# Performance work log

Hardware: AMD Instinct MI355X
Metric: run time of the kernel (lower is better)

The kernel has to match this reference:

```python
import jax, jax.numpy as jnp
import numpy as np

DIM = 128
HEADS = 4
OUT = DIM // HEADS  # 32
NEG_SLOPE = 0.2
EPS = 1e-16


def setup_inputs() -> dict:
    key = jax.random.key(0)
    k1, k2, k3, k4, k5, k6 = jax.random.split(key, 6)
    B, T, E = 4, 4096, 131072
    x = jax.random.normal(k1, (B, T, DIM), dtype=jnp.float32)
    edge_index = jax.random.randint(k2, (2, E), 0, T, dtype=jnp.int64)
    # GATConv params (PyG layout): lin weight [heads*out, in], att [heads, out], bias [heads*out]
    W = jax.random.normal(k3, (HEADS * OUT, DIM), dtype=jnp.float32) / np.sqrt(DIM)
    att_src = jax.random.normal(k4, (HEADS, OUT), dtype=jnp.float32) / np.sqrt(OUT)
    att_dst = jax.random.normal(k5, (HEADS, OUT), dtype=jnp.float32) / np.sqrt(OUT)
    bias = jax.random.normal(k6, (HEADS * OUT,), dtype=jnp.float32) * 0.01
    return {"x": x, "edge_index": edge_index, "W": W, "att_src": att_src, "att_dst": att_dst, "bias": bias}


def reference(x, edge_index, W, att_src, att_dst, bias):
    B, T, D = x.shape
    N = B * T
    E = edge_index.shape[1]
    # batch the temporal edge list: repeat(1, B) + per-graph node offset b*T
    offsets = jnp.repeat(jnp.arange(B, dtype=edge_index.dtype) * T, E)
    src = jnp.tile(edge_index[0], B) + offsets
    dst = jnp.tile(edge_index[1], B) + offsets
    # PyG GATConv default add_self_loops=True
    loops = jnp.arange(N, dtype=edge_index.dtype)
    src = jnp.concatenate([src, loops])
    dst = jnp.concatenate([dst, loops])

    h = (x.reshape(N, D) @ W.T).reshape(N, HEADS, OUT)          # [N,H,O]
    a_src = jnp.einsum('nho,ho->nh', h, att_src)                # [N,H]
    a_dst = jnp.einsum('nho,ho->nh', h, att_dst)

    e = a_src[src] + a_dst[dst]                                  # [Etot,H]
    e = jax.nn.leaky_relu(e, NEG_SLOPE)
    # segment softmax over destination neighborhoods
    m = jax.ops.segment_max(e, dst, num_segments=N)              # [N,H]
    ex = jnp.exp(e - m[dst])
    s = jax.ops.segment_sum(ex, dst, num_segments=N)
    alpha = ex / (s[dst] + EPS)                                  # [Etot,H]

    msg = h[src] * alpha[:, :, None]                             # [Etot,H,O]
    out = jax.ops.segment_sum(msg, dst, num_segments=N)          # [N,H,O]
    out = out.reshape(N, HEADS * OUT) + bias
    return out.reshape(B, T, D)
```

## Files before the change

kernel.cpp:

```cpp
#include <hip/hip_runtime.h>

#define TPG   4096
#define NHEAD 4
#define DIMD  128
#define NEG   0.2f

__device__ __forceinline__ int load_edge(const void* ei, int is64, long idx) {
  if (is64) return (int)((const long long*)ei)[idx];
  return ((const int*)ei)[idx];
}

__device__ __forceinline__ int detect64_block(const unsigned* __restrict__ ei) {
  __shared__ int s64;
  int t = threadIdx.x;
  if (t == 0) s64 = 1;
  __syncthreads();
  if (t < 256) {
    unsigned v = ei[2 * t + 1];
    if (v != 0u) s64 = 0;
  }
  __syncthreads();
  return s64;
}

__global__ __launch_bounds__(256) void k_gemm(
    const float* __restrict__ x, const float* __restrict__ W,
    const float* __restrict__ atts, const float* __restrict__ attd,
    float* __restrict__ h, float* __restrict__ as_n, float* __restrict__ ad_n,
    int* __restrict__ counts) {
  __shared__ float4 xs4[16][33];
  int t = threadIdx.x;
  if (blockIdx.x < 16) counts[(blockIdx.x << 8) + t] = 0;
  int base = blockIdx.x * 16;
  const float4* x4 = (const float4*)x;
  for (int i = t; i < 512; i += 256) {
    xs4[i >> 5][i & 31] = x4[base * 32 + i];
  }
  __syncthreads();

  int n_sub = t & 15, cgrp = t >> 4;
  int c0 = cgrp * 8;
  const float4* W4 = (const float4*)W;
  float acc[8];
#pragma unroll
  for (int k = 0; k < 8; ++k) acc[k] = 0.f;

  for (int db = 0; db < 32; db += 8) {
    float4 xa[8];
#pragma unroll
    for (int i = 0; i < 8; ++i) xa[i] = xs4[n_sub][db + i];
#pragma unroll
    for (int k = 0; k < 8; ++k) {
      const float4* wr = W4 + (c0 + k) * 32 + db;
      float a = acc[k];
#pragma unroll
      for (int i = 0; i < 8; ++i) {
        float4 w = wr[i];
        a = fmaf(xa[i].x, w.x, a);
        a = fmaf(xa[i].y, w.y, a);
        a = fmaf(xa[i].z, w.z, a);
        a = fmaf(xa[i].w, w.w, a);
      }
      acc[k] = a;
    }
  }

  int n = base + n_sub;
  float4* hp = (float4*)(h + (n << 7) + c0);
  hp[0] = make_float4(acc[0], acc[1], acc[2], acc[3]);
  hp[1] = make_float4(acc[4], acc[5], acc[6], acc[7]);

  float ps = 0.f, pd = 0.f;
#pragma unroll
  for (int k = 0; k < 8; ++k) {
    ps = fmaf(acc[k], atts[c0 + k], ps);
    pd = fmaf(acc[k], attd[c0 + k], pd);
  }
  ps += __shfl_xor(ps, 16); ps += __shfl_xor(ps, 32);
  pd += __shfl_xor(pd, 16); pd += __shfl_xor(pd, 32);
  if ((t & 48) == 0) {
    as_n[(n << 2) + (t >> 6)] = ps;
    ad_n[(n << 2) + (t >> 6)] = pd;
  }
}

__global__ __launch_bounds__(256) void k_hist(const void* __restrict__ ei,
                                              int* __restrict__ counts, int E) {
  int is64 = detect64_block((const unsigned*)ei);
  int e = blockIdx.x * blockDim.x + threadIdx.x;
  if (e >= E) return;
  int dst = load_edge(ei, is64, (long)E + e);
  atomicAdd(&counts[dst], 1);
}

__global__ __launch_bounds__(1024) void k_scan(const int* __restrict__ counts,
                                               int* __restrict__ offs,
                                               int* __restrict__ cursor) {
  __shared__ int wsum[16];
  __shared__ int woff[17];
  int t = threadIdx.x;
  int b = t * 4;
  int v0 = counts[b], v1 = counts[b + 1], v2 = counts[b + 2], v3 = counts[b + 3];
  int s0 = v0 + v1 + v2 + v3;
  int lane = t & 63, w = t >> 6;
  int sc = s0;
#pragma unroll
  for (int off = 1; off < 64; off <<= 1) {
    int o = __shfl_up(sc, off);
    if (lane >= off) sc += o;
  }
  if (lane == 63) wsum[w] = sc;
  __syncthreads();
  if (t == 0) {
    int a = 0;
#pragma unroll
    for (int i = 0; i < 16; ++i) { woff[i] = a; a += wsum[i]; }
    woff[16] = a;
  }
  __syncthreads();
  int a = woff[w] + sc - s0;
  offs[b] = a;     cursor[b] = a;     a += v0;
  offs[b + 1] = a; cursor[b + 1] = a; a += v1;
  offs[b + 2] = a; cursor[b + 2] = a; a += v2;
  offs[b + 3] = a; cursor[b + 3] = a;
  if (t == 1023) offs[4096] = woff[16];
}

__global__ __launch_bounds__(256) void k_scatter(const void* __restrict__ ei,
                                                 int* __restrict__ cursor,
                                                 int* __restrict__ esrc, int E) {
  int is64 = detect64_block((const unsigned*)ei);
  int e = blockIdx.x * blockDim.x + threadIdx.x;
  if (e >= E) return;
  int src = load_edge(ei, is64, e);
  int dst = load_edge(ei, is64, (long)E + e);
  int pos = atomicAdd(&cursor[dst], 1);
  esrc[pos] = src;
}

__global__ __launch_bounds__(256) void k_aggr(
    const int* __restrict__ offs, const int* __restrict__ esrc,
    const float* __restrict__ h, const float* __restrict__ as_n,
    const float* __restrict__ ad_n, const float* __restrict__ bias,
    float* __restrict__ out) {
  int lane = threadIdx.x & 63;
  int n = __builtin_amdgcn_readfirstlane((blockIdx.x << 2) + (threadIdx.x >> 6));
  int tloc = n & (TPG - 1);
  int nodebase = n - tloc;
  int beg = __builtin_amdgcn_readfirstlane(offs[tloc]);
  int end = __builtin_amdgcn_readfirstlane(offs[tloc + 1]);

  int myh = lane >> 4;
  int c = lane << 1;
  float adst = ad_n[(n << 2) + myh];

  float m, s;
  float2 acc;
  {
    float e = as_n[(n << 2) + myh] + adst;
    e = e > 0.f ? e : NEG * e;
    m = e; s = 1.f;
    acc = *(const float2*)(h + ((size_t)n << 7) + c);
  }

  for (int j0 = beg; j0 < end; j0 += 8) {
    int sgk[8];
#pragma unroll
    for (int k = 0; k < 8; ++k) {
      int j = j0 + k;
      sgk[k] = (j < end) ? (nodebase + esrc[j]) : n;
    }
    float ek[8];
#pragma unroll
    for (int k = 0; k < 8; ++k) {
      float e = as_n[((size_t)sgk[k] << 2) + myh] + adst;
      e = e > 0.f ? e : NEG * e;
      ek[k] = (j0 + k < end) ? e : -1e30f;
    }
    float2 hv[8];
#pragma unroll
    for (int k = 0; k < 8; ++k)
      hv[k] = *(const float2*)(h + ((size_t)sgk[k] << 7) + c);

    float bm = ek[0];
#pragma unroll
    for (int k = 1; k < 8; ++k) bm = fmaxf(bm, ek[k]);
    float mn = fmaxf(m, bm);
    float r = __expf(m - mn);
    float ps = 0.f, px = 0.f, py = 0.f;
#pragma unroll
    for (int k = 0; k < 8; ++k) {
      float al = __expf(ek[k] - mn);
      ps += al;
      px = fmaf(al, hv[k].x, px);
      py = fmaf(al, hv[k].y, py);
    }
    acc.x = fmaf(acc.x, r, px);
    acc.y = fmaf(acc.y, r, py);
    s = fmaf(s, r, ps);
    m = mn;
  }

  float invs = 1.f / (s + 1e-16f);
  const float2 bi = *(const float2*)(bias + c);
  float2 o;
  o.x = fmaf(acc.x, invs, bi.x);
  o.y = fmaf(acc.y, invs, bi.y);
  *(float2*)(out + ((size_t)n << 7) + c) = o;
}

extern "C" void kernel_launch(void* const* d_in, const int* in_sizes, int n_in,
                              void* d_out, int out_size, void* d_ws, size_t ws_size,
                              hipStream_t stream) {
  const float* x    = (const float*)d_in[0];
  const void*  ei   = d_in[1];
  const float* W    = (const float*)d_in[2];
  const float* atts = (const float*)d_in[3];
  const float* attd = (const float*)d_in[4];
  const float* bias = (const float*)d_in[5];
  float* out = (float*)d_out;

  int N = in_sizes[0] / DIMD;
  int E = in_sizes[1] / 2;

  char* p = (char*)d_ws;
  float* h      = (float*)p; p += (size_t)N * DIMD * 4;
  float* as_n   = (float*)p; p += (size_t)N * NHEAD * 4;
  float* ad_n   = (float*)p; p += (size_t)N * NHEAD * 4;
  int*   counts = (int*)p;   p += (size_t)TPG * 4;
  int*   offs   = (int*)p;   p += (size_t)(TPG + 1) * 4;
  int*   cursor = (int*)p;   p += (size_t)TPG * 4;
  int*   esrc   = (int*)p;   p += (size_t)E * 4;

  k_gemm<<<N / 16, 256, 0, stream>>>(x, W, atts, attd, h, as_n, ad_n, counts);
  k_hist<<<(E + 255) / 256, 256, 0, stream>>>(ei, counts, E);
  k_scan<<<1, 1024, 0, stream>>>(counts, offs, cursor);
  k_scatter<<<(E + 255) / 256, 256, 0, stream>>>(ei, cursor, esrc, E);
  k_aggr<<<N / 4, 256, 0, stream>>>(offs, esrc, h, as_n, ad_n, bias, out);
}
```

Before: 153.2 us.

## Fuse histogram and scan via last-block pattern, remap aggregation to two waves per node

The separate scan launch is folded into the histogram kernel: the last block to finish, detected through an atomic counter reset in the GEMM kernel, performs the prefix sum over destination counts. The aggregation kernel now uses two wavefronts per node, each handling two heads with one float per lane instead of float2. Blocks are remapped so that each batch graph's nodes are grouped onto a pair of XCDs, aiming at better L2 locality for h gathers. This removes one launch and raises parallelism, at the cost of more redundant index/logit loads per node and a serialized tail block for the scan.

Result: slower. 170.6 us (+11.4%).

```diff
diff --git a/kernel.cpp b/kernel.cpp
--- a/kernel.cpp
+++ b/kernel.cpp
@@ -27,10 +27,11 @@
     const float* __restrict__ x, const float* __restrict__ W,
     const float* __restrict__ atts, const float* __restrict__ attd,
     float* __restrict__ h, float* __restrict__ as_n, float* __restrict__ ad_n,
-    int* __restrict__ counts) {
+    int* __restrict__ counts, int* __restrict__ done) {
   __shared__ float4 xs4[16][33];
   int t = threadIdx.x;
   if (blockIdx.x < 16) counts[(blockIdx.x << 8) + t] = 0;
+  if (blockIdx.x == 16 && t == 0) *done = 0;
   int base = blockIdx.x * 16;
   const float4* x4 = (const float4*)x;
   for (int i = t; i < 512; i += 256) {
@@ -66,7 +67,7 @@
   }
 
   int n = base + n_sub;
-  float4* hp = (float4*)(h + (n << 7) + c0);
+  float4* hp = (float4*)(h + ((size_t)n << 7) + c0);
   hp[0] = make_float4(acc[0], acc[1], acc[2], acc[3]);
   hp[1] = make_float4(acc[4], acc[5], acc[6], acc[7]);
 
@@ -84,46 +85,48 @@
   }
 }
 
-__global__ __launch_bounds__(256) void k_hist(const void* __restrict__ ei,
-                                              int* __restrict__ counts, int E) {
+__global__ __launch_bounds__(256) void k_histscan(
+    const void* __restrict__ ei, int* __restrict__ counts,
+    int* __restrict__ offs, int* __restrict__ cursor,
+    int* __restrict__ done, int E) {
   int is64 = detect64_block((const unsigned*)ei);
-  int e = blockIdx.x * blockDim.x + threadIdx.x;
-  if (e >= E) return;
-  int dst = load_edge(ei, is64, (long)E + e);
-  atomicAdd(&counts[dst], 1);
-}
-
-__global__ __launch_bounds__(1024) void k_scan(const int* __restrict__ counts,
-                                               int* __restrict__ offs,
-                                               int* __restrict__ cursor) {
-  __shared__ int wsum[16];
-  __shared__ int woff[17];
   int t = threadIdx.x;
-  int b = t * 4;
-  int v0 = counts[b], v1 = counts[b + 1], v2 = counts[b + 2], v3 = counts[b + 3];
-  int s0 = v0 + v1 + v2 + v3;
+  int e = blockIdx.x * 256 + t;
+  if (e < E) {
+    int dst = load_edge(ei, is64, (long)E + e);
+    atomicAdd(&counts[dst], 1);
+  }
+  __syncthreads();
+  __shared__ int lastFlag;
+  if (t == 0) {
+    __threadfence();
+    int prev = atomicAdd(done, 1);
+    lastFlag = (prev == (int)gridDim.x - 1);
+  }
+  __syncthreads();
+  if (!lastFlag) return;
+
+  int v[16]; int sum = 0;
+#pragma unroll
+  for (int i = 0; i < 16; ++i) { v[i] = atomicAdd(&counts[t * 16 + i], 0); sum += v[i]; }
   int lane = t & 63, w = t >> 6;
-  int sc = s0;
+  int sc = sum;
 #pragma unroll
   for (int off = 1; off < 64; off <<= 1) {
     int o = __shfl_up(sc, off);
     if (lane >= off) sc += o;
   }
+  __shared__ int wsum[4];
   if (lane == 63) wsum[w] = sc;
   __syncthreads();
-  if (t == 0) {
-    int a = 0;
-#pragma unroll
-    for (int i = 0; i < 16; ++i) { woff[i] = a; a += wsum[i]; }
-    woff[16] = a;
-  }
-  __syncthreads();
-  int a = woff[w] + sc - s0;
-  offs[b] = a;     cursor[b] = a;     a += v0;
-  offs[b + 1] = a; cursor[b + 1] = a; a += v1;
-  offs[b + 2] = a; cursor[b + 2] = a; a += v2;
-  offs[b + 3] = a; cursor[b + 3] = a;
-  if (t == 1023) offs[4096] = woff[16];
+  int wo = 0;
+  for (int i = 0; i < w; ++i) wo += wsum[i];
+  int a = wo + sc - sum;
+#pragma unroll
+  for (int i = 0; i < 16; ++i) {
+    offs[t * 16 + i] = a; cursor[t * 16 + i] = a; a += v[i];
+  }
+  if (t == 255) offs[4096] = a;
 }
 
 __global__ __launch_bounds__(256) void k_scatter(const void* __restrict__ ei,
@@ -143,24 +146,30 @@
     const float* __restrict__ h, const float* __restrict__ as_n,
     const float* __restrict__ ad_n, const float* __restrict__ bias,
     float* __restrict__ out) {
+  int bid = blockIdx.x;
+  int wv = threadIdx.x >> 6;
   int lane = threadIdx.x & 63;
-  int n = __builtin_amdgcn_readfirstlane((blockIdx.x << 2) + (threadIdx.x >> 6));
+  int xcd = bid & 7, slot = bid >> 3;
+  int g = xcd >> 1, pair = xcd & 1;
+  int group = (slot << 1) + pair;
+  int n = (g << 12) + (group << 1) + (wv >> 1);
+  n = __builtin_amdgcn_readfirstlane(n);
+  int hpair = wv & 1;
   int tloc = n & (TPG - 1);
   int nodebase = n - tloc;
   int beg = __builtin_amdgcn_readfirstlane(offs[tloc]);
   int end = __builtin_amdgcn_readfirstlane(offs[tloc + 1]);
 
-  int myh = lane >> 4;
-  int c = lane << 1;
-  float adst = ad_n[(n << 2) + myh];
-
-  float m, s;
-  float2 acc;
+  int hh = (hpair << 1) + (lane >> 5);
+  int ch = (hh << 5) + (lane & 31);
+  float adst = ad_n[(n << 2) + hh];
+
+  float m, s, acc;
   {
-    float e = as_n[(n << 2) + myh] + adst;
+    float e = as_n[(n << 2) + hh] + adst;
     e = e > 0.f ? e : NEG * e;
     m = e; s = 1.f;
-    acc = *(const float2*)(h + ((size_t)n << 7) + c);
+    acc = h[((size_t)n << 7) + ch];
   }
 
   for (int j0 = beg; j0 < end; j0 += 8) {
@@ -170,43 +179,34 @@
       int j = j0 + k;
       sgk[k] = (j < end) ? (nodebase + esrc[j]) : n;
     }
+    float hv[8];
+#pragma unroll
+    for (int k = 0; k < 8; ++k) hv[k] = h[((size_t)sgk[k] << 7) + ch];
     float ek[8];
 #pragma unroll
     for (int k = 0; k < 8; ++k) {
-      float e = as_n[((size_t)sgk[k] << 2) + myh] + adst;
+      float e = as_n[(sgk[k] << 2) + hh] + adst;
       e = e > 0.f ? e : NEG * e;
       ek[k] = (j0 + k < end) ? e : -1e30f;
     }
-    float2 hv[8];
-#pragma unroll
-    for (int k = 0; k < 8; ++k)
-      hv[k] = *(const float2*)(h + ((size_t)sgk[k] << 7) + c);
-
-    float bm = ek[0];
-#pragma unroll
-    for (int k = 1; k < 8; ++k) bm = fmaxf(bm, ek[k]);
+    float bm = fmaxf(fmaxf(fmaxf(ek[0], ek[1]), fmaxf(ek[2], ek[3])),
+                     fmaxf(fmaxf(ek[4], ek[5]), fmaxf(ek[6], ek[7])));
     float mn = fmaxf(m, bm);
     float r = __expf(m - mn);
-    float ps = 0.f, px = 0.f, py = 0.f;
+    float ps = 0.f, pa = 0.f;
 #pragma unroll
     for (int k = 0; k < 8; ++k) {
       float al = __expf(ek[k] - mn);
       ps += al;
-      px = fmaf(al, hv[k].x, px);
-      py = fmaf(al, hv[k].y, py);
-    }
-    acc.x = fmaf(acc.x, r, px);
-    acc.y = fmaf(acc.y, r, py);
+      pa = fmaf(al, hv[k], pa);
+    }
+    acc = fmaf(acc, r, pa);
     s = fmaf(s, r, ps);
     m = mn;
   }
 
   float invs = 1.f / (s + 1e-16f);
-  const float2 bi = *(const float2*)(bias + c);
-  float2 o;
-  o.x = fmaf(acc.x, invs, bi.x);
-  o.y = fmaf(acc.y, invs, bi.y);
-  *(float2*)(out + ((size_t)n << 7) + c) = o;
+  out[((size_t)n << 7) + ch] = fmaf(acc, invs, bias[ch]);
 }
 
 extern "C" void kernel_launch(void* const* d_in, const int* in_sizes, int n_in,
@@ -231,10 +231,10 @@
   int*   offs   = (int*)p;   p += (size_t)(TPG + 1) * 4;
   int*   cursor = (int*)p;   p += (size_t)TPG * 4;
   int*   esrc   = (int*)p;   p += (size_t)E * 4;
-
-  k_gemm<<<N / 16, 256, 0, stream>>>(x, W, atts, attd, h, as_n, ad_n, counts);
-  k_hist<<<(E + 255) / 256, 256, 0, stream>>>(ei, counts, E);
-  k_scan<<<1, 1024, 0, stream>>>(counts, offs, cursor);
+  int*   done   = (int*)p;   p += 4;
+
+  k_gemm<<<N / 16, 256, 0, stream>>>(x, W, atts, attd, h, as_n, ad_n, counts, done);
+  k_histscan<<<(E + 255) / 256, 256, 0, stream>>>(ei, counts, offs, cursor, done, E);
   k_scatter<<<(E + 255) / 256, 256, 0, stream>>>(ei, cursor, esrc, E);
-  k_aggr<<<N / 4, 256, 0, stream>>>(offs, esrc, h, as_n, ad_n, bias, out);
-}
+  k_aggr<<<N / 2, 256, 0, stream>>>(offs, esrc, h, as_n, ad_n, bias, out);
+}
```
